# Optimization experiments

Hardware: AMD Instinct MI355X
Metric: run time of the kernel (lower is better)

Reference implementation:

```python
import jax, jax.numpy as jnp
import numpy as np
from jax import lax

B = 128
IM = 56  # im_size: 56 -> 48 -> 20 -> 6 spatial, 256*6*6/8 = 1152 primary capsules


def _conv(x, w, b, stride):
    y = lax.conv_general_dilated(x, w, (stride, stride), 'VALID',
                                 dimension_numbers=('NCHW', 'OIHW', 'NCHW'))
    return y + b[None, :, None, None]


def _squash(t, eps=1e-8):
    sn = jnp.sum(t * t, axis=-1, keepdims=True)
    return (sn / (1.0 + sn)) * t / jnp.sqrt(sn + eps)


def setup_inputs() -> dict:
    key = jax.random.key(0)
    ks = jax.random.split(key, 9)
    s = 0.02
    f32 = jnp.float32
    return {
        'x': jax.random.normal(ks[0], (B, 1, IM, IM), f32),
        'conv1_w': jax.random.normal(ks[1], (256, 1, 9, 9), f32) * s,
        'conv1_b': jnp.zeros((256,), f32),
        'conv2_w': jax.random.normal(ks[2], (256, 256, 9, 9), f32) * s,
        'conv2_b': jnp.zeros((256,), f32),
        'prim_w': jax.random.normal(ks[3], (256, 256, 9, 9), f32) * s,
        'prim_b': jnp.zeros((256,), f32),
        'W_digit': jax.random.normal(ks[4], (10, 1152, 8, 16), f32) * s,  # Linear(9216,16) per digit, reshaped
        'b_digit': jnp.zeros((10, 16), f32),
        'rec_w1': jax.random.normal(ks[5], (160, 512), f32) * s,
        'rec_b1': jnp.zeros((512,), f32),
        'rec_w2': jax.random.normal(ks[6], (512, 1024), f32) * s,
        'rec_b2': jnp.zeros((1024,), f32),
        'rec_w3': jax.random.normal(ks[7], (1024, IM * IM), f32) * s,
        'rec_b3': jnp.zeros((IM * IM,), f32),
    }


def reference(x, conv1_w, conv1_b, conv2_w, conv2_b, prim_w, prim_b,
              W_digit, b_digit, rec_w1, rec_b1, rec_w2, rec_b2, rec_w3, rec_b3):
    out = jax.nn.relu(_conv(x, conv1_w, conv1_b, 1))    # [B,256,48,48]
    out = jax.nn.relu(_conv(out, conv2_w, conv2_b, 2))  # [B,256,20,20]
    out = jax.nn.relu(_conv(out, prim_w, prim_b, 2))    # [B,256,6,6]
    u = _squash(out.reshape(out.shape[0], -1, 8))       # [B,1152,8]
    # fused 10-way digit-capsule transform: u_hat[b,i,j,:] = W[j,i] @ u[b,i]
    u_hat = jnp.einsum('bid,jido->bijo', u, W_digit)    # [B,1152,10,16]
    b_ij = jnp.zeros(u_hat.shape[:3], u_hat.dtype)      # [B,1152,10]
    num_iterations = 3
    v = None
    for it in range(num_iterations):
        c = jax.nn.softmax(b_ij, axis=1)                       # coupling over input capsules
        s_j = jnp.einsum('bij,bijo->bjo', c, u_hat) + b_digit  # [B,10,16]
        v = _squash(s_j)
        if it < num_iterations - 1:
            b_ij = b_ij + jnp.einsum('bijo,bjo->bij', u_hat, v)
    rec = v.reshape(v.shape[0], -1)                     # [B,160]
    rec = jax.nn.relu(rec @ rec_w1 + rec_b1)
    rec = jax.nn.relu(rec @ rec_w2 + rec_b2)
    rec = jax.nn.sigmoid(rec @ rec_w3 + rec_b3)         # [B,3136]
    return (v, rec)
```

## Files before the change

kernel.cpp:

```cpp
#include <hip/hip_runtime.h>
#include <hip/hip_bf16.h>

typedef float f32x4 __attribute__((ext_vector_type(4)));
typedef __bf16 bf16x8 __attribute__((ext_vector_type(8)));
typedef __bf16 bf16x4 __attribute__((ext_vector_type(4)));
typedef int i32x8 __attribute__((ext_vector_type(8)));

#define AS1 __attribute__((address_space(1)))
#define AS3 __attribute__((address_space(3)))

__device__ __forceinline__ void gload16(const void* g, void* l) {
    __builtin_amdgcn_global_load_lds((AS1 unsigned int*)g, (AS3 unsigned int*)l, 16, 0, 0);
}

__device__ __forceinline__ float bfu(unsigned short u) {
    return __uint_as_float((unsigned)u << 16);
}

__device__ __forceinline__ unsigned char f2e4m3s(float f) {
    unsigned u = __float_as_uint(f);
    unsigned s = (u >> 24) & 0x80;
    unsigned ua = u & 0x7fffffffu;
    int e = (int)(ua >> 23) - 127;
    unsigned m = (ua >> 20) & 7;
    if (e < -6) return (unsigned char)s;
    if (e > 8 || (e == 8 && m > 6)) return (unsigned char)(s | 0x7e);
    return (unsigned char)(s | ((unsigned)(e + 7) << 3) | m);
}

__global__ __launch_bounds__(256) void prep_w_kernel(const float* __restrict__ pw,
                                                     __hip_bfloat16* __restrict__ w3p,
                                                     const float* __restrict__ c1w,
                                                     __hip_bfloat16* __restrict__ wb,
                                                     const float* __restrict__ x,
                                                     __hip_bfloat16* __restrict__ xb,
                                                     const float* __restrict__ c2w,
                                                     unsigned char* __restrict__ wq2) {
    int bid = blockIdx.x;
    int t = threadIdx.x;
    if (bid == 512) {
        float tmp[81];
#pragma unroll
        for (int k = 0; k < 81; ++k) tmp[k] = c1w[t * 81 + k];
#pragma unroll
        for (int ks = 0; ks < 9; ++ks)
#pragma unroll
            for (int e = 0; e < 8; ++e)
                wb[(ks * 256 + t) * 8 + e] = __float2bfloat16(tmp[ks * 9 + e]);
#pragma unroll
        for (int e = 0; e < 8; ++e)
            wb[(9 * 256 + t) * 8 + e] = __float2bfloat16(tmp[e * 9 + 8]);
        wb[(10 * 256 + t) * 8 + 0] = __float2bfloat16(tmp[80]);
#pragma unroll
        for (int e = 1; e < 8; ++e) wb[(10 * 256 + t) * 8 + e] = __float2bfloat16(0.f);
#pragma unroll
        for (int e = 0; e < 8; ++e) wb[(11 * 256 + t) * 8 + e] = __float2bfloat16(0.f);
        return;
    }
    if (bid >= 513 && bid < 905) {
        long i4 = (long)(bid - 513) * 1024 + t * 4;
        float4 v = *(const float4*)(x + i4);
        bf16x4 o = {(__bf16)v.x, (__bf16)v.y, (__bf16)v.z, (__bf16)v.w};
        *(bf16x4*)((__bf16*)xb + i4) = o;
        return;
    }
    if (bid >= 905) {
        int b2 = bid - 905;
        int icg = b2 / 42; int rem = b2 - icg * 42;
        int ks = rem >> 1, nblk = rem & 1;
        long base = (long)icg * 688128 + (long)ks * 32768 + (long)nblk * 16384;
#pragma unroll
        for (int u = 0; u < 64; ++u) {
            int flat = t * 64 + u;
            int ocl = flat >> 7, kb = flat & 127;
            int kq = kb >> 5, icl = kb & 31;
            int kyx = ks * 4 + kq;
            float v = 0.f;
            if (kyx < 81)
                v = c2w[(long)(nblk * 128 + ocl) * 20736 + (icg * 32 + icl) * 81 + kyx] * 64.f;
            wq2[base + flat] = f2e4m3s(v);
        }
        return;
    }
    __shared__ float wl[4 * 32 * 81];
    int icg = bid & 7;
    int oc4 = (bid >> 3) & 31;
    int nblk = bid >> 8;
    int ocg0 = nblk * 128 + oc4 * 4;
    int ic0 = icg * 32;
    for (int f = t; f < 4 * 2592; f += 256) {
        int o = f / 2592;
        int rest = f - o * 2592;
        wl[f] = pw[(ocg0 + o) * 20736 + ic0 * 81 + rest];
    }
    __syncthreads();
    for (int idx = t; idx < 81 * 128; idx += 256) {
        int kyx = idx >> 7;
        int o = (idx >> 5) & 3;
        int i = idx & 31;
        long dst = (long)(((kyx * 8 + icg) * 2 + nblk) * 128 + (oc4 * 4 + o)) * 32 + i;
        w3p[dst] = __float2bfloat16(wl[o * 2592 + i * 81 + kyx]);
    }
}

__global__ __launch_bounds__(256) void conv1_mfma_kernel(const __hip_bfloat16* __restrict__ xb,
                                                         const __hip_bfloat16* __restrict__ wb,
                                                         const float* __restrict__ bias,
                                                         unsigned char* __restrict__ out) {
    __shared__ __bf16 Asl[640];
    int bid = blockIdx.x;
    int b = bid / 24, mb2 = bid - b * 24;
    int oy0 = mb2 * 2;
    int t = threadIdx.x;
    int lane = t & 63, wc = t >> 6;
    int q = lane >> 4;

    const __bf16* src = (const __bf16*)xb + b * 3136 + oy0 * 56;
    for (int idx = t; idx < 640; idx += 256) {
        int iy = idx >> 6, col = idx & 63;
        Asl[idx] = (col < 56) ? src[iy * 56 + col] : (__bf16)0.f;
    }

    bf16x8 Bf[3][4];
#pragma unroll
    for (int s = 0; s < 3; ++s)
#pragma unroll
        for (int ni = 0; ni < 4; ++ni) {
            int col = wc * 64 + ni * 16 + (lane & 15);
            Bf[s][ni] = *(const bf16x8*)(wb + ((s * 4 + q) * 256 + col) * 8);
        }

    f32x4 acc[6][4];
#pragma unroll
    for (int i = 0; i < 6; ++i)
#pragma unroll
        for (int j = 0; j < 4; ++j) acc[i][j] = (f32x4){0.f, 0.f, 0.f, 0.f};

    __syncthreads();

#pragma unroll
    for (int s = 0; s < 3; ++s) {
        int ks = s * 4 + q;
        bf16x8 af[6];
#pragma unroll
        for (int mi = 0; mi < 6; ++mi) {
            int r = mi * 16 + (lane & 15);
            int oyl = (r >= 48) ? 1 : 0;
            int ox = r - 48 * oyl;
            bf16x8 v;
            if (ks < 9) {
                __builtin_memcpy(&v, &Asl[(oyl + ks) * 64 + ox], 16);
            } else if (ks == 9) {
#pragma unroll
                for (int e = 0; e < 8; ++e) v[e] = Asl[(oyl + e) * 64 + ox + 8];
            } else if (ks == 10) {
#pragma unroll
                for (int e = 0; e < 8; ++e) v[e] = (__bf16)0.f;
                v[0] = Asl[(oyl + 8) * 64 + ox + 8];
            } else {
#pragma unroll
                for (int e = 0; e < 8; ++e) v[e] = (__bf16)0.f;
            }
            af[mi] = v;
        }
#pragma unroll
        for (int mi = 0; mi < 6; ++mi)
#pragma unroll
            for (int ni = 0; ni < 4; ++ni)
                acc[mi][ni] = __builtin_amdgcn_mfma_f32_16x16x32_bf16(af[mi], Bf[s][ni], acc[mi][ni], 0, 0, 0);
    }

    long m0 = (long)b * 2304 + mb2 * 96;
#pragma unroll
    for (int mi = 0; mi < 6; ++mi)
#pragma unroll
        for (int ni = 0; ni < 4; ++ni) {
            int col = wc * 64 + ni * 16 + (lane & 15);
            float bs = bias[col];
#pragma unroll
            for (int r2 = 0; r2 < 4; ++r2) {
                int row = mi * 16 + q * 4 + r2;
                float vv = acc[mi][ni][r2] + bs;
                vv = vv > 0.f ? vv : 0.f;
                out[(m0 + row) * 256 + col] = f2e4m3s(vv * 16.f);
            }
        }
}

__global__ __launch_bounds__(512, 2) void conv2_fp8_kernel(const unsigned char* __restrict__ in,
                                                           const unsigned char* __restrict__ wq,
                                                           const float* __restrict__ bias,
                                                           __hip_bfloat16* __restrict__ out) {
    __shared__ unsigned char Ald[75264];
    int bid = blockIdx.x;
    int wg = (bid & 7) * 32 + (bid >> 3);
    int b = wg >> 1, nblk = wg & 1;
    int t = threadIdx.x;
    int lane = t & 63, wid = t >> 6;
    int wr = wid >> 1, wc = wid & 1;
    int kq = lane >> 4;

    const unsigned char* imgbase = in + (long)b * (48 * 48 * 256);
    const unsigned char* wqn = wq + ((long)(nblk * 128 + wc * 64 + (lane & 15))) * 128 + kq * 32;

    int qrow[7];
#pragma unroll
    for (int mi = 0; mi < 7; ++mi) {
        int ml = wr * 96 + mi * 16 + (lane & 15);
        int oy = ml / 20, ox = ml - oy * 20;
        qrow[mi] = ((2 * oy) * 49 + 2 * ox) * 32;
    }

    f32x4 acc[7][4];
#pragma unroll
    for (int i = 0; i < 7; ++i)
#pragma unroll
        for (int j = 0; j < 4; ++j) acc[i][j] = (f32x4){0.f, 0.f, 0.f, 0.f};

    auto stageA = [&](int icg) {
#pragma unroll 3
        for (int j = 0; j < 9; ++j) {
            int gi = t + j * 512;
            int row32 = gi >> 1, half = gi & 1;
            int iy = row32 / 48, col = row32 - iy * 48;
            uint4 v = *(const uint4*)(imgbase + ((long)(iy * 48 + col) * 256 + icg * 32 + half * 16));
            *(uint4*)(Ald + (iy * 49 + col) * 32 + half * 16) = v;
        }
    };

    union U8 { uint4 q[2]; i32x8 v; };
    i32x8 Be[4], Bo[4];
    auto loadB = [&](i32x8* dst, int icg, int ks) {
        const unsigned char* p = wqn + (long)icg * 688128 + (long)ks * 32768;
        uint4* d = (uint4*)dst;
#pragma unroll
        for (int ni = 0; ni < 4; ++ni) {
            d[ni * 2]     = *(const uint4*)(p + ni * 2048);
            d[ni * 2 + 1] = *(const uint4*)(p + ni * 2048 + 16);
        }
    };

    auto step = [&](int icg, int ks, i32x8* Bcur, i32x8* Bnxt) {
        if (ks + 1 < 21) loadB(Bnxt, icg, ks + 1);
        int kyx = ks * 4 + kq;
        int ky = kyx / 9;
        int kdel = (kyx + 40 * ky) * 32;
        __builtin_amdgcn_s_setprio(1);
#pragma unroll
        for (int mi = 0; mi < 7; ++mi) {
            const unsigned char* ap = Ald + qrow[mi] + kdel;
            U8 a;
            a.q[0] = *(const uint4*)ap;
            a.q[1] = *(const uint4*)(ap + 16);
#pragma unroll
            for (int ni = 0; ni < 4; ++ni)
                acc[mi][ni] = __builtin_amdgcn_mfma_scale_f32_16x16x128_f8f6f4(
                    a.v, Bcur[ni], acc[mi][ni],
                    0, 0,
                    0, 0x7F7F7F7F,
                    0, 0x7F7F7F7F);
        }
        __builtin_amdgcn_s_setprio(0);
    };

    for (int icg = 0; icg < 8; ++icg) {
        if (icg) __builtin_amdgcn_s_barrier();
        loadB(Be, icg, 0);
        stageA(icg);
        asm volatile("s_waitcnt lgkmcnt(0)" ::: "memory");
        __builtin_amdgcn_s_barrier();
        if (wid >= 4) asm volatile("s_sleep 4");
        for (int kk = 0; kk < 10; ++kk) {
            step(icg, 2 * kk, Be, Bo);
            step(icg, 2 * kk + 1, Bo, Be);
        }
        step(icg, 20, Be, Bo);
    }

    int colbase = nblk * 128 + wc * 64 + (lane & 15);
    const float inv = 1.f / 1024.f;
#pragma unroll
    for (int mi = 0; mi < 7; ++mi) {
#pragma unroll
        for (int ni = 0; ni < 4; ++ni) {
            int col = colbase + ni * 16;
            float bs = bias[col];
#pragma unroll
            for (int r = 0; r < 4; ++r) {
                int ml = wr * 96 + mi * 16 + (lane >> 4) * 4 + r;
                float v = acc[mi][ni][r] * inv + bs;
                v = v > 0.f ? v : 0.f;
                out[((long)b * 400 + ml) * 256 + col] = __float2bfloat16(v);
            }
        }
    }
}

__global__ __launch_bounds__(256) void conv_mfma_kernel(const __hip_bfloat16* __restrict__ in,
                                                        const __hip_bfloat16* __restrict__ wp,
                                                        const float* __restrict__ bias,
                                                        __hip_bfloat16* __restrict__ out,
                                                        __hip_bfloat16* __restrict__ part,
                                                        int Win, int imgStride, int HWout, int Wout,
                                                        int nkyx, int Mtot, int mode) {
    __shared__ __hip_bfloat16 Ald[3 * 4096];
    __shared__ __hip_bfloat16 Bld[3 * 4096];
    int mblk = blockIdx.x, nblk = blockIdx.y;
    int kyx0 = blockIdx.z * nkyx;
    int t = threadIdx.x;
    int lane = t & 63, wid = t >> 6;
    int swz = ((t & 3) ^ ((t >> 3) & 3)) * 8;
    int icsrc = swz;
    long bsrc = (t >> 2) * 32 + swz;

    long base0, base1;
    {
        int m = mblk * 128 + (t >> 2);
        int b = m / HWout; int rem = m - b * HWout;
        int oyy = rem / Wout; int oxx = rem - oyy * Wout;
        base0 = (long)b * imgStride + (long)(2 * oyy * Win + 2 * oxx) * 256;
        m += 64;
        b = m / HWout; rem = m - b * HWout;
        oyy = rem / Wout; oxx = rem - oyy * Wout;
        base1 = (long)b * imgStride + (long)(2 * oyy * Win + 2 * oxx) * 256;
    }

    f32x4 acc[4][4];
#pragma unroll
    for (int i = 0; i < 4; ++i)
#pragma unroll
        for (int j2 = 0; j2 < 4; ++j2) acc[i][j2] = (f32x4){0.f, 0.f, 0.f, 0.f};

    int wr = wid >> 1, wc = wid & 1;
    int slot8 = (((lane >> 4) ^ ((lane >> 1) & 3))) * 8;
    int a_off = ((wr * 64 + (lane & 15)) * 32 + slot8) * 2;
    int b_off = ((wc * 64 + (lane & 15)) * 32 + slot8) * 2;

    auto stage = [&](int s, int buf) {
        int kyx = kyx0 + (s >> 3);
        int icg = s & 7;
        int ky = kyx / 9, kx = kyx - ky * 9;
        long offA = (long)(ky * Win + kx) * 256 + icg * 32 + icsrc;
        long btb = (long)((kyx * 8 + icg) * 2 + nblk) * 4096 + bsrc;
        char* a0 = (char*)Ald + buf * 8192 + wid * 1024;
        char* b0 = (char*)Bld + buf * 8192 + wid * 1024;
        gload16(in + base0 + offA, a0);
        gload16(in + base1 + offA, a0 + 4096);
        gload16(wp + btb, b0);
        gload16(wp + btb + 2048, b0 + 4096);
    };

    int nsteps = nkyx * 8;
    stage(0, 0);
    stage(1, 1);
    stage(2, 2);
    int cur = 0;
    for (int s = 0; s < nsteps; ++s) {
        int rem = nsteps - 1 - s;
        if (rem >= 2) {
            asm volatile("s_waitcnt vmcnt(8)" ::: "memory");
        } else if (rem == 1) {
            asm volatile("s_waitcnt vmcnt(4)" ::: "memory");
        } else {
            asm volatile("s_waitcnt vmcnt(0)" ::: "memory");
        }
        __builtin_amdgcn_s_barrier();
        __builtin_amdgcn_sched_barrier(0);
        const char* Ac = (const char*)Ald + cur * 8192;
        const char* Bc = (const char*)Bld + cur * 8192;
        bf16x8 af[4], bfr[4];
#pragma unroll
        for (int i = 0; i < 4; ++i) af[i] = *(const bf16x8*)(Ac + a_off + i * 1024);
#pragma unroll
        for (int i = 0; i < 4; ++i) bfr[i] = *(const bf16x8*)(Bc + b_off + i * 1024);
#pragma unroll
        for (int mi = 0; mi < 4; ++mi)
#pragma unroll
            for (int ni = 0; ni < 4; ++ni)
                acc[mi][ni] = __builtin_amdgcn_mfma_f32_16x16x32_bf16(af[mi], bfr[ni], acc[mi][ni], 0, 0, 0);
        if (s + 3 < nsteps) {
            asm volatile("s_waitcnt lgkmcnt(0)" ::: "memory");
            __builtin_amdgcn_s_barrier();
            stage(s + 3, cur);
        }
        cur = (cur == 2) ? 0 : cur + 1;
    }

    int colbase = nblk * 128 + wc * 64 + (lane & 15);
    long mrowbase = (long)mblk * 128 + wr * 64 + (lane >> 4) * 4;
    if (mode == 0) {
#pragma unroll
        for (int mi = 0; mi < 4; ++mi) {
#pragma unroll
            for (int ni = 0; ni < 4; ++ni) {
                int col = colbase + ni * 16;
                float bs = bias[col];
#pragma unroll
                for (int r = 0; r < 4; ++r) {
                    long mrow = mrowbase + mi * 16 + r;
                    float v = acc[mi][ni][r] + bs;
                    v = v > 0.f ? v : 0.f;
                    out[mrow * 256 + col] = __float2bfloat16(v);
                }
            }
        }
    } else {
        __hip_bfloat16* pp = part + (long)blockIdx.z * Mtot * 256;
#pragma unroll
        for (int mi = 0; mi < 4; ++mi) {
#pragma unroll
            for (int ni = 0; ni < 4; ++ni) {
                int col = colbase + ni * 16;
#pragma unroll
                for (int r = 0; r < 4; ++r) {
                    long mrow = mrowbase + mi * 16 + r;
                    pp[mrow * 256 + col] = __float2bfloat16(acc[mi][ni][r]);
                }
            }
        }
    }
}

__global__ __launch_bounds__(256) void reduce_parts_kernel(const __hip_bfloat16* __restrict__ part,
                                                           const float* __restrict__ bias,
                                                           __hip_bfloat16* __restrict__ out) {
    int idx = blockIdx.x * 256 + threadIdx.x;
    float s = 0.f;
#pragma unroll
    for (int p = 0; p < 9; ++p) s += __bfloat162float(part[(long)p * 1179648 + idx]);
    s += bias[idx & 255];
    s = s > 0.f ? s : 0.f;
    out[idx] = __float2bfloat16(s);
}

__global__ __launch_bounds__(256) void squash_caps_kernel(const __hip_bfloat16* __restrict__ c3,
                                                          float* __restrict__ uT) {
    int g = blockIdx.x * 256 + threadIdx.x;
    int i = g >> 7, b = g & 127;
    float val[8];
    float sn = 0.f;
#pragma unroll
    for (int d = 0; d < 8; ++d) {
        int flat = i * 8 + d;
        int c = flat / 36; int rem = flat - c * 36;
        int y = rem / 6; int xx = rem - y * 6;
        float vv = __bfloat162float(c3[((b * 6 + y) * 6 + xx) * 256 + c]);
        val[d] = vv;
        sn += vv * vv;
    }
    float sc = (sn / (1.f + sn)) / sqrtf(sn + 1e-8f);
#pragma unroll
    for (int d = 0; d < 8; ++d) uT[(long)g * 8 + d] = val[d] * sc;
}

__global__ __launch_bounds__(256) void uhat_kernel(const float* __restrict__ uT,
                                                   const float* __restrict__ Wd,
                                                   __hip_bfloat16* __restrict__ uhat) {
    __shared__ float Wl2[1600];
    __shared__ float ul[1024];
    int i = blockIdx.x, t = threadIdx.x;
    for (int idx = t; idx < 1280; idx += 256) {
        int j = idx >> 7, rest = idx & 127;
        int d = rest >> 4, o = rest & 15;
        Wl2[(j * 16 + o) * 10 + d] = Wd[((long)j * 1152 + i) * 128 + rest];
    }
    {
        const float4* usrc = (const float4*)(uT + (long)i * 1024);
        float4* ud = (float4*)ul;
        ud[t] = usrc[t];
    }
    __syncthreads();
    int b = (t >= 160) ? 1 : 0;
    int jo = (t >= 160) ? t - 160 : t;
    for (int rr = 0; rr < 80; ++rr) {
        const float* up = &ul[b * 8];
        const float* wq = &Wl2[jo * 10];
        float a = 0.f;
#pragma unroll
        for (int d = 0; d < 8; ++d) a += up[d] * wq[d];
        int j = jo >> 4, o = jo & 15;
        uhat[(((long)b * 10 + j) * 1152 + i) * 16 + o] = __float2bfloat16(a);
        jo += 96; b += 1;
        if (jo >= 160) { jo -= 160; b += 1; }
    }
}

__global__ __launch_bounds__(256) void routing_kernel(const __hip_bfloat16* __restrict__ uhat,
                                                      const float* __restrict__ bdig,
                                                      float* __restrict__ vout,
                                                      float* __restrict__ vws) {
    __shared__ __hip_bfloat16 uh[1152 * 16];
    __shared__ float barr[1152];
    __shared__ float red[16];
    __shared__ float accb[16 * 256];
    __shared__ float svec[16];
    __shared__ float vsc[16];
    int bid = blockIdx.x;
    int j = bid % 10;
    int t = threadIdx.x;
    int wid = t >> 6;
    const uint4* srcp = (const uint4*)(uhat + (long)bid * 18432);
    uint4* dstp = (uint4*)uh;
    for (int idx = t; idx < 2304; idx += 256) dstp[idx] = srcp[idx];
    for (int idx = t; idx < 1152; idx += 256) barr[idx] = 0.f;
    __syncthreads();
    for (int it = 0; it < 3; ++it) {
        float lm = -1e30f;
        for (int i = t; i < 1152; i += 256) lm = fmaxf(lm, barr[i]);
#pragma unroll
        for (int m2 = 32; m2; m2 >>= 1) lm = fmaxf(lm, __shfl_xor(lm, m2));
        if ((t & 63) == 0) red[wid] = lm;
        __syncthreads();
        float mx = fmaxf(fmaxf(red[0], red[1]), fmaxf(red[2], red[3]));
        float le = 0.f;
        float a16[16];
#pragma unroll
        for (int o = 0; o < 16; ++o) a16[o] = 0.f;
        for (int i = t; i < 1152; i += 256) {
            float e = __expf(barr[i] - mx);
            le += e;
            const uint4* up = (const uint4*)(uh + i * 16);
            union { uint4 q; unsigned short s[8]; } U0, U1;
            U0.q = up[0]; U1.q = up[1];
#pragma unroll
            for (int o = 0; o < 8; ++o) a16[o] += e * bfu(U0.s[o]);
#pragma unroll
            for (int o = 0; o < 8; ++o) a16[8 + o] += e * bfu(U1.s[o]);
        }
#pragma unroll
        for (int m2 = 32; m2; m2 >>= 1) le += __shfl_xor(le, m2);
        if ((t & 63) == 0) red[4 + wid] = le;
#pragma unroll
        for (int o = 0; o < 16; ++o) accb[o * 256 + t] = a16[o];
        __syncthreads();
        float sume = red[4] + red[5] + red[6] + red[7];
        int g = t >> 4, tin = t & 15;
        float s = 0.f;
#pragma unroll
        for (int k = 0; k < 16; ++k) s += accb[g * 256 + tin + 16 * k];
#pragma unroll
        for (int m2 = 8; m2; m2 >>= 1) s += __shfl_xor(s, m2);
        if (tin == 0) svec[g] = s / sume + bdig[j * 16 + g];
        __syncthreads();
        if (t < 16) {
            float sv = svec[t];
            float sn = sv * sv;
#pragma unroll
            for (int m2 = 8; m2; m2 >>= 1) sn += __shfl_xor(sn, m2);
            float sc = (sn / (1.f + sn)) / sqrtf(sn + 1e-8f);
            float v = sv * sc;
            vsc[t] = v;
            if (it == 2) { vout[bid * 16 + t] = v; vws[bid * 16 + t] = v; }
        }
        __syncthreads();
        if (it < 2) {
            for (int i = t; i < 1152; i += 256) {
                const uint4* up = (const uint4*)(uh + i * 16);
                union { uint4 q; unsigned short s[8]; } U0, U1;
                U0.q = up[0]; U1.q = up[1];
                float dot = 0.f;
#pragma unroll
                for (int o = 0; o < 8; ++o) dot += vsc[o] * bfu(U0.s[o]);
#pragma unroll
                for (int o = 0; o < 8; ++o) dot += vsc[8 + o] * bfu(U1.s[o]);
                barr[i] += dot;
            }
            __syncthreads();
        }
    }
}

__global__ __launch_bounds__(256) void rec_gemm_kernel(const float* __restrict__ A,
                                                       const float* __restrict__ W,
                                                       const float* __restrict__ bias,
                                                       float* __restrict__ out,
                                                       int K, int N, int act) {
    __shared__ __align__(16) float As[2][2048];
    int n0 = blockIdx.x * 64;
    int bch = blockIdx.y * 32;
    int t = threadIdx.x;
    int n_l = t & 63, bh = t >> 6;
    const float* Wc = W + n0 + n_l;
    float acc[8];
#pragma unroll
    for (int i = 0; i < 8; ++i) acc[i] = 0.f;
    int T = (K + 63) >> 6;

    auto stageA = [&](int tile, int buf) {
        int k0 = tile << 6;
        for (int idx = t; idx < 2048; idx += 256) {
            int bb = idx >> 6, kk = idx & 63;
            As[buf][idx] = (k0 + kk < K) ? A[(long)(bch + bb) * K + k0 + kk] : 0.f;
        }
    };
    auto ldW = [&](int tile, float* w) {
        int k0 = tile << 6;
#pragma unroll
        for (int j = 0; j < 64; ++j) {
            int kr = k0 + j;
            if (kr >= K) kr = K - 1;
            w[j] = Wc[(long)kr * N];
        }
    };
    auto compute = [&](const float* w, int buf) {
#pragma unroll
        for (int bb = 0; bb < 8; ++bb) {
            const float4* ap = (const float4*)&As[buf][(bh * 8 + bb) * 64];
            float s = 0.f;
#pragma unroll
            for (int q = 0; q < 16; ++q) {
                float4 a = ap[q];
                s += a.x * w[q * 4] + a.y * w[q * 4 + 1] + a.z * w[q * 4 + 2] + a.w * w[q * 4 + 3];
            }
            acc[bb] += s;
        }
    };

    float wA[64], wB[64];
    ldW(0, wA);
    stageA(0, 0);
    __syncthreads();
    for (int tile = 0; tile < T; tile += 2) {
        if (tile + 1 < T) { ldW(tile + 1, wB); stageA(tile + 1, 1); }
        compute(wA, 0);
        __syncthreads();
        if (tile + 1 < T) {
            if (tile + 2 < T) { ldW(tile + 2, wA); stageA(tile + 2, 0); }
            compute(wB, 1);
            __syncthreads();
        }
    }

    float bs = bias[n0 + n_l];
#pragma unroll
    for (int bb = 0; bb < 8; ++bb) {
        float x = acc[bb] + bs;
        float r;
        if (act == 0) r = x > 0.f ? x : 0.f;
        else r = 1.f / (1.f + __expf(-x));
        out[(long)(bch + bh * 8 + bb) * N + n0 + n_l] = r;
    }
}

extern "C" void kernel_launch(void* const* d_in, const int* in_sizes, int n_in,
                              void* d_out, int out_size, void* d_ws, size_t ws_size,
                              hipStream_t stream) {
    const float* x   = (const float*)d_in[0];
    const float* c1w = (const float*)d_in[1];
    const float* c1b = (const float*)d_in[2];
    const float* c2w = (const float*)d_in[3];
    const float* c2b = (const float*)d_in[4];
    const float* pw  = (const float*)d_in[5];
    const float* pb  = (const float*)d_in[6];
    const float* Wd  = (const float*)d_in[7];
    const float* bd  = (const float*)d_in[8];
    const float* rw1 = (const float*)d_in[9];
    const float* rb1 = (const float*)d_in[10];
    const float* rw2 = (const float*)d_in[11];
    const float* rb2 = (const float*)d_in[12];
    const float* rw3 = (const float*)d_in[13];
    const float* rb3 = (const float*)d_in[14];
    float* outp = (float*)d_out;

    char* ws = (char*)d_ws;
    size_t off = 0;
    auto alloc = [&](size_t bytes) {
        char* p = ws + off;
        off += (bytes + 255) & ~(size_t)255;
        return p;
    };
    unsigned char* c1f8  = (unsigned char*)alloc(75497472UL);
    __hip_bfloat16* c2out = (__hip_bfloat16*)alloc(26214400UL);
    __hip_bfloat16* c3out = (__hip_bfloat16*)alloc(2359296UL);
    __hip_bfloat16* w3p   = (__hip_bfloat16*)alloc(10616832UL);
    unsigned char* wq2    = (unsigned char*)alloc(5505024UL);
    __hip_bfloat16* xb    = (__hip_bfloat16*)alloc(802816UL);
    __hip_bfloat16* wb    = (__hip_bfloat16*)alloc(49152UL);
    float* uT    = (float*)alloc(4718592UL);
    __hip_bfloat16* uhat = (__hip_bfloat16*)alloc(47185920UL);
    float* vws   = (float*)alloc(81920UL);
    float* rec1  = (float*)alloc(262144UL);
    float* rec2  = (float*)alloc(524288UL);

    __hip_bfloat16* c3part = (__hip_bfloat16*)uhat;

    prep_w_kernel<<<1241, 256, 0, stream>>>(pw, w3p, c1w, wb, x, xb, c2w, wq2);
    conv1_mfma_kernel<<<3072, 256, 0, stream>>>(xb, wb, c1b, c1f8);
    conv2_fp8_kernel<<<256, 512, 0, stream>>>(c1f8, wq2, c2b, c2out);
    conv_mfma_kernel<<<dim3(36, 2, 9), 256, 0, stream>>>(c2out, w3p, pb, c3out, c3part,
                                                         20, 20 * 20 * 256, 36, 6, 9, 4608, 1);
    reduce_parts_kernel<<<4608, 256, 0, stream>>>(c3part, pb, c3out);
    squash_caps_kernel<<<576, 256, 0, stream>>>(c3out, uT);
    uhat_kernel<<<1152, 256, 0, stream>>>(uT, Wd, uhat);
    routing_kernel<<<1280, 256, 0, stream>>>(uhat, bd, outp, vws);
    rec_gemm_kernel<<<dim3(8, 4), 256, 0, stream>>>(vws, rw1, rb1, rec1, 160, 512, 0);
    rec_gemm_kernel<<<dim3(16, 4), 256, 0, stream>>>(rec1, rw2, rb2, rec2, 512, 1024, 0);
    rec_gemm_kernel<<<dim3(49, 4), 256, 0, stream>>>(rec2, rw3, rb3, outp + 20480, 1024, 3136, 1);
}
```

Before: 785.2 us.

## Swizzle conv2 LDS activation layout and stage FP8 weight prep through shared memory

The conv2 FP8 kernel's LDS activation tile now uses an XOR swizzle on 16-byte slots. Stores in stageA and the paired A-fragment reads in the MFMA loop both use the swizzled address, which is meant to reduce LDS bank conflicts. The FP8 weight-quantization part of prep_w_kernel now loads contiguous 4-output-channel slabs into shared memory before transposing, replacing scattered global reads. The grid grows from 1241 to 1417 blocks to match, and each A-fragment read now costs extra integer ops to compute the swizzled address.

New measurement: 775.9 us. No clear change (-1.2%).

```diff
diff --git a/kernel.cpp b/kernel.cpp
--- a/kernel.cpp
+++ b/kernel.cpp
@@ -65,24 +65,30 @@
         return;
     }
     if (bid >= 905) {
+        __shared__ float wl[4 * 2592];
         int b2 = bid - 905;
-        int icg = b2 / 42; int rem = b2 - icg * 42;
-        int ks = rem >> 1, nblk = rem & 1;
-        long base = (long)icg * 688128 + (long)ks * 32768 + (long)nblk * 16384;
-#pragma unroll
-        for (int u = 0; u < 64; ++u) {
-            int flat = t * 64 + u;
-            int ocl = flat >> 7, kb = flat & 127;
+        int icg = b2 & 7;
+        int oc4 = (b2 >> 3) & 31;
+        int nblk = b2 >> 8;
+        for (int f = t; f < 4 * 2592; f += 256) {
+            int o = f / 2592;
+            int rest = f - o * 2592;
+            wl[f] = c2w[(long)(nblk * 128 + oc4 * 4 + o) * 20736 + icg * 2592 + rest];
+        }
+        __syncthreads();
+        long base = (long)icg * 688128 + (long)nblk * 16384 + (oc4 * 4) * 128;
+        for (int idx = t; idx < 4 * 21 * 128; idx += 256) {
+            int o = idx / 2688;
+            int rem = idx - o * 2688;
+            int ks = rem >> 7, kb = rem & 127;
             int kq = kb >> 5, icl = kb & 31;
             int kyx = ks * 4 + kq;
-            float v = 0.f;
-            if (kyx < 81)
-                v = c2w[(long)(nblk * 128 + ocl) * 20736 + (icg * 32 + icl) * 81 + kyx] * 64.f;
-            wq2[base + flat] = f2e4m3s(v);
+            float v = (kyx < 81) ? wl[o * 2592 + icl * 81 + kyx] * 64.f : 0.f;
+            wq2[base + (long)ks * 32768 + o * 128 + kb] = f2e4m3s(v);
         }
         return;
     }
-    __shared__ float wl[4 * 32 * 81];
+    __shared__ float wl3[4 * 32 * 81];
     int icg = bid & 7;
     int oc4 = (bid >> 3) & 31;
     int nblk = bid >> 8;
@@ -91,7 +97,7 @@
     for (int f = t; f < 4 * 2592; f += 256) {
         int o = f / 2592;
         int rest = f - o * 2592;
-        wl[f] = pw[(ocg0 + o) * 20736 + ic0 * 81 + rest];
+        wl3[f] = pw[(ocg0 + o) * 20736 + ic0 * 81 + rest];
     }
     __syncthreads();
     for (int idx = t; idx < 81 * 128; idx += 256) {
@@ -99,7 +105,7 @@
         int o = (idx >> 5) & 3;
         int i = idx & 31;
         long dst = (long)(((kyx * 8 + icg) * 2 + nblk) * 128 + (oc4 * 4 + o)) * 32 + i;
-        w3p[dst] = __float2bfloat16(wl[o * 2592 + i * 81 + kyx]);
+        w3p[dst] = __float2bfloat16(wl3[o * 2592 + i * 81 + kyx]);
     }
 }
 
@@ -203,12 +209,12 @@
     const unsigned char* imgbase = in + (long)b * (48 * 48 * 256);
     const unsigned char* wqn = wq + ((long)(nblk * 128 + wc * 64 + (lane & 15))) * 128 + kq * 32;
 
-    int qrow[7];
+    int qslot[7];
 #pragma unroll
     for (int mi = 0; mi < 7; ++mi) {
         int ml = wr * 96 + mi * 16 + (lane & 15);
         int oy = ml / 20, ox = ml - oy * 20;
-        qrow[mi] = ((2 * oy) * 49 + 2 * ox) * 32;
+        qslot[mi] = ((2 * oy) * 49 + 2 * ox) * 2;
     }
 
     f32x4 acc[7][4];
@@ -224,7 +230,9 @@
             int row32 = gi >> 1, half = gi & 1;
             int iy = row32 / 48, col = row32 - iy * 48;
             uint4 v = *(const uint4*)(imgbase + ((long)(iy * 48 + col) * 256 + icg * 32 + half * 16));
-            *(uint4*)(Ald + (iy * 49 + col) * 32 + half * 16) = v;
+            int slot = (iy * 49 + col) * 2 + half;
+            int phys = slot ^ ((slot >> 3) & 7);
+            *(uint4*)(Ald + phys * 16) = v;
         }
     };
 
@@ -244,14 +252,17 @@
         if (ks + 1 < 21) loadB(Bnxt, icg, ks + 1);
         int kyx = ks * 4 + kq;
         int ky = kyx / 9;
-        int kdel = (kyx + 40 * ky) * 32;
+        int sdel = (kyx + 40 * ky) * 2;
         __builtin_amdgcn_s_setprio(1);
 #pragma unroll
         for (int mi = 0; mi < 7; ++mi) {
-            const unsigned char* ap = Ald + qrow[mi] + kdel;
+            int s0 = qslot[mi] + sdel;
+            int p0 = s0 ^ ((s0 >> 3) & 7);
+            int s1 = s0 + 1;
+            int p1 = s1 ^ ((s1 >> 3) & 7);
             U8 a;
-            a.q[0] = *(const uint4*)ap;
-            a.q[1] = *(const uint4*)(ap + 16);
+            a.q[0] = *(const uint4*)(Ald + p0 * 16);
+            a.q[1] = *(const uint4*)(Ald + p1 * 16);
 #pragma unroll
             for (int ni = 0; ni < 4; ++ni)
                 acc[mi][ni] = __builtin_amdgcn_mfma_scale_f32_16x16x128_f8f6f4(
@@ -684,7 +695,7 @@
 
     __hip_bfloat16* c3part = (__hip_bfloat16*)uhat;
 
-    prep_w_kernel<<<1241, 256, 0, stream>>>(pw, w3p, c1w, wb, x, xb, c2w, wq2);
+    prep_w_kernel<<<1417, 256, 0, stream>>>(pw, w3p, c1w, wb, x, xb, c2w, wq2);
     conv1_mfma_kernel<<<3072, 256, 0, stream>>>(xb, wb, c1b, c1f8);
     conv2_fp8_kernel<<<256, 512, 0, stream>>>(c1f8, wq2, c2b, c2out);
     conv_mfma_kernel<<<dim3(36, 2, 9), 256, 0, stream>>>(c2out, w3p, pb, c3out, c3part,
```
